# Kernel tuning notes

Hardware: AMD Instinct MI355X
Metric: run time of the kernel (lower is better)

## Reference

```python
import jax, jax.numpy as jnp
import numpy as np

MIN_C = 1e-6
MIN_NORM = 1e-15
BALL_EPS = 0.004  # float32 ball epsilon


def _norm(x):
    return jnp.maximum(jnp.linalg.norm(x, axis=-1, keepdims=True), MIN_NORM)


def _project(x, c):
    norm = _norm(x)
    maxnorm = (1.0 - BALL_EPS) / jnp.sqrt(c)
    return jnp.where(norm > maxnorm, x / norm * maxnorm, x)


def _tanh(x):
    return jnp.tanh(jnp.clip(x, -15.0, 15.0))


def _artanh(x):
    x = jnp.clip(x, -1.0 + 1e-5, 1.0 - 1e-5)
    return 0.5 * (jnp.log1p(x) - jnp.log1p(-x))


def _expmap0(u, c):
    sc = jnp.sqrt(c)
    n = _norm(u)
    return _project(_tanh(sc * n) * u / (sc * n), c)


def _logmap0(y, c):
    sc = jnp.sqrt(c)
    n = _norm(y)
    return y / n / sc * _artanh(sc * n)


def _mobius_add(x, y, c):
    x2 = jnp.sum(x * x, -1, keepdims=True)
    y2 = jnp.sum(y * y, -1, keepdims=True)
    xy = jnp.sum(x * y, -1, keepdims=True)
    num = (1 + 2 * c * xy + c * y2) * x + (1 - c * x2) * y
    den = jnp.maximum(1 + 2 * c * xy + c * c * x2 * y2, MIN_NORM)
    return num / den


N_NODE, N_EDGE, D, ATTN, B, N_VOCAB = 100000, 1000000, 64, 64, 256, 401


def setup_inputs() -> dict:
    key = jax.random.key(0)
    ks = jax.random.split(key, 12)
    r_idx = jax.random.randint(ks[0], (N_EDGE,), 0, B, dtype=jnp.int32)
    rel = jax.random.randint(ks[1], (N_EDGE,), 0, N_VOCAB, dtype=jnp.int32)
    sub = jax.random.randint(ks[2], (N_EDGE,), 0, N_NODE, dtype=jnp.int32)
    obj = jax.random.randint(ks[3], (N_EDGE,), 0, N_NODE, dtype=jnp.int32)
    zero = jnp.zeros((N_EDGE,), jnp.int32)
    edges = jnp.stack([r_idx, zero, rel, zero, sub, obj], axis=1)  # [E, 6]
    s = 0.1
    return {
        "hidden": jax.random.normal(ks[4], (N_NODE, D), jnp.float32) * s,
        "q_rel": jax.random.randint(ks[5], (B,), 0, N_VOCAB, dtype=jnp.int32),
        "edges": edges,
        "rela_embed": jax.random.normal(ks[6], (N_VOCAB, D), jnp.float32) * s,
        "Ws_w": jax.random.normal(ks[7], (ATTN, D), jnp.float32) * s,
        "Wr_w": jax.random.normal(ks[8], (ATTN, D), jnp.float32) * s,
        "Wqr_w": jax.random.normal(ks[9], (ATTN, D), jnp.float32) * s,
        "Wqr_b": jnp.zeros((ATTN,), jnp.float32),
        "Wattn_w": jax.random.normal(ks[10], (1, ATTN), jnp.float32) * s,
        "Wh_w": jax.random.normal(ks[11], (D, D), jnp.float32) * s,
        "n_node": N_NODE,
    }


def reference(hidden, q_rel, edges, rela_embed, Ws_w, Wr_w, Wqr_w, Wqr_b, Wattn_w, Wh_w, n_node):
    c = MIN_C
    sub, rel, obj, r_idx = edges[:, 4], edges[:, 2], edges[:, 5], edges[:, 0]
    hs = hidden[sub]                 # [E, D] gather
    hr = rela_embed[rel]             # [E, D]
    h_qr = rela_embed[q_rel][r_idx]  # [E, D]
    # attention MLP -> scalar gate per edge
    pre = hs @ Ws_w.T + hr @ Wr_w.T + h_qr @ Wqr_w.T + Wqr_b
    alpha = jax.nn.sigmoid(jax.nn.relu(pre) @ Wattn_w.T)  # [E, 1]
    # hyperbolic message
    hs_h = _expmap0(hs, c)
    hr_h = _expmap0(hr, c)
    mess2 = _logmap0(_project(_mobius_add(hs_h, hr_h, c), c), c)
    message = mess2 * alpha
    agg = jax.ops.segment_sum(message, obj, num_segments=n_node)  # scatter-add
    a = _expmap0(agg @ Wh_w.T, c)
    a = jax.nn.relu(a)  # act
    return _logmap0(a, c)
```

## Files before the change

### kernel.cpp

```cpp
#include <hip/hip_runtime.h>
#include <math.h>
#include <stdint.h>

#define N_NODE 100000
#define N_EDGE 1000000
#define DIM    64
#define NB     256
#define NVOCAB 401
#define SCAN_B 1024
#define NCHUNK ((N_NODE + SCAN_B - 1) / SCAN_B)
#define AGG_WAVES 8192

typedef short short8  __attribute__((ext_vector_type(8)));
typedef float floatx4 __attribute__((ext_vector_type(4)));
typedef unsigned short ushort_t;

__device__ inline unsigned short f2bf_rne(float f)
{
    unsigned u = __float_as_uint(f);
    unsigned r = u + 0x7FFF + ((u >> 16) & 1);
    return (unsigned short)(r >> 16);
}
__device__ inline float bflo(unsigned u) { return __uint_as_float(u << 16); }
__device__ inline float bfhi(unsigned u) { return __uint_as_float(u & 0xFFFF0000u); }
__device__ inline unsigned short f2h(float f)
{
    _Float16 h = (_Float16)f;
    unsigned short s; __builtin_memcpy(&s, &h, 2); return s;
}
__device__ inline float h2f(unsigned b)
{
    unsigned short s = (unsigned short)b;
    _Float16 h; __builtin_memcpy(&h, &s, 2); return (float)h;
}

__device__ inline void split8(float4 v0, float4 v1, short8& hi, short8& lo)
{
    float f[8] = {v0.x, v0.y, v0.z, v0.w, v1.x, v1.y, v1.z, v1.w};
    #pragma unroll
    for (int j = 0; j < 8; ++j) {
        unsigned u = __float_as_uint(f[j]);
        unsigned r = u + 0x7FFF + ((u >> 16) & 1);
        unsigned short h = (unsigned short)(r >> 16);
        float hf = __uint_as_float(((unsigned)h) << 16);
        float l  = f[j] - hf;
        unsigned u2 = __float_as_uint(l);
        unsigned r2 = u2 + 0x7FFF + ((u2 >> 16) & 1);
        hi[j] = (short)h;
        lo[j] = (short)(r2 >> 16);
    }
}

__device__ void gemm64_body(
    const float* __restrict__ X,
    const int*   __restrict__ idx,
    const float* __restrict__ W,
    const float* __restrict__ bias,
    void* __restrict__ Yv,
    ushort_t* __restrict__ Y2,
    int R, int out_mode, int blk)
{
    int wave = threadIdx.x >> 6;
    int lane = threadIdx.x & 63;
    int m    = lane & 15;
    int quad = lane >> 4;
    int r0   = blk * 64 + wave * 16;

    int r = r0 + m;
    int src = (r < R) ? (idx ? idx[r] : r) : 0;
    const float* xrow = X + (size_t)src * DIM + quad * 8;

    float4 a0[2], a1[2];
    #pragma unroll
    for (int c = 0; c < 2; ++c) {
        a0[c] = *(const float4*)(xrow + 32 * c);
        a1[c] = *(const float4*)(xrow + 32 * c + 4);
    }
    short8 ah[2], al[2];
    #pragma unroll
    for (int c = 0; c < 2; ++c) split8(a0[c], a1[c], ah[c], al[c]);

    if (out_mode == 3 && r < R) {
        #pragma unroll
        for (int c = 0; c < 2; ++c)
            *(short8*)(Y2 + (size_t)r * DIM + 32 * c + quad * 8) = ah[c];
    }

    floatx4 acc[4] = {{0,0,0,0},{0,0,0,0},{0,0,0,0},{0,0,0,0}};
    #pragma unroll
    for (int g = 0; g < 4; ++g) {
        const float* wrow = W + (size_t)(g * 16 + m) * DIM + quad * 8;
        #pragma unroll
        for (int c = 0; c < 2; ++c) {
            float4 b0 = *(const float4*)(wrow + 32 * c);
            float4 b1 = *(const float4*)(wrow + 32 * c + 4);
            short8 bh, bl;
            split8(b0, b1, bh, bl);
            acc[g] = __builtin_amdgcn_mfma_f32_16x16x32_bf16(ah[c], bh, acc[g], 0, 0, 0);
            acc[g] = __builtin_amdgcn_mfma_f32_16x16x32_bf16(ah[c], bl, acc[g], 0, 0, 0);
            acc[g] = __builtin_amdgcn_mfma_f32_16x16x32_bf16(al[c], bh, acc[g], 0, 0, 0);
        }
    }

    #pragma unroll
    for (int g = 0; g < 4; ++g) {
        float bv = bias ? bias[g * 16 + m] : 0.0f;
        #pragma unroll
        for (int reg = 0; reg < 4; ++reg) {
            int rr = r0 + quad * 4 + reg;
            if (rr < R) {
                float v = acc[g][reg] + bv;
                if (out_mode == 1) v = fmaxf(v, 0.0f);
                if (out_mode >= 2)
                    ((ushort_t*)Yv)[(size_t)rr * DIM + g * 16 + m] = f2bf_rne(v);
                else
                    ((float*)Yv)[(size_t)rr * DIM + g * 16 + m] = v;
            }
        }
    }
}

__global__ __launch_bounds__(256) void gemm64_kernel(
    const float* __restrict__ X,
    const int*   __restrict__ idx,
    const float* __restrict__ W,
    const float* __restrict__ bias,
    void* __restrict__ Yv,
    ushort_t* __restrict__ Y2,
    int R, int out_mode)
{
    gemm64_body(X, idx, W, bias, Yv, Y2, R, out_mode, blockIdx.x);
}

#define G1 ((N_NODE + 63) / 64)
#define G2 ((NVOCAB + 63) / 64)
#define G3 (NB / 64)
#define GSMALL (G2 + G3)
#define GD4 ((N_EDGE + 1023) / 1024)
#define PREP_T (G1 + GD4)
#define PREP_GRID (GSMALL + PREP_T)

__global__ __launch_bounds__(256) void prep_kernel(
    const float* __restrict__ hidden,
    const float* __restrict__ rela,
    const int*   __restrict__ q_rel,
    const float* __restrict__ Ws,
    const float* __restrict__ Wr,
    const float* __restrict__ Wqr,
    const float* __restrict__ Wqr_b,
    ushort_t* __restrict__ hsWs,
    ushort_t* __restrict__ hidb,
    ushort_t* __restrict__ rel_preb,
    ushort_t* __restrict__ relab,
    ushort_t* __restrict__ qr_preb,
    const int* __restrict__ edges,
    int* __restrict__ deg,
    int* __restrict__ rank)
{
    int b = blockIdx.x;
    if (b < G2) {
        gemm64_body(rela, nullptr, Wr, nullptr, rel_preb, relab, NVOCAB, 3, b);
    } else if (b < GSMALL) {
        gemm64_body(rela, q_rel, Wqr, Wqr_b, qr_preb, nullptr, NB, 2, b - G2);
    } else {
        int bp = b - GSMALL;
        int prior = (int)(((long)bp * GD4) / PREP_T);
        int nxt   = (int)(((long)(bp + 1) * GD4) / PREP_T);
        if (nxt > prior) {
            int base = prior * 1024 + threadIdx.x;
            #pragma unroll
            for (int k = 0; k < 4; ++k) {
                int e = base + k * 256;
                if (e < N_EDGE) {
                    int2 so = *(const int2*)(edges + (size_t)e * 6 + 4);
                    rank[e] = atomicAdd(&deg[so.y], 1);
                }
            }
        } else {
            gemm64_body(hidden, nullptr, Ws, nullptr, hsWs, hidb, N_NODE, 3, bp - prior);
        }
    }
}

__global__ __launch_bounds__(SCAN_B) void scan1_kernel(const int* __restrict__ deg,
                                                       int* __restrict__ partial)
{
    __shared__ int s[SCAN_B];
    int g = blockIdx.x * SCAN_B + threadIdx.x;
    s[threadIdx.x] = (g < N_NODE) ? deg[g] : 0;
    __syncthreads();
    for (int off = SCAN_B / 2; off; off >>= 1) {
        if (threadIdx.x < off) s[threadIdx.x] += s[threadIdx.x + off];
        __syncthreads();
    }
    if (threadIdx.x == 0) partial[blockIdx.x] = s[0];
}

__global__ __launch_bounds__(128) void scan2_kernel(int* __restrict__ partial, int n)
{
    __shared__ int s[128];
    int t = threadIdx.x;
    int v = (t < n) ? partial[t] : 0;
    s[t] = v;
    __syncthreads();
    for (int off = 1; off < 128; off <<= 1) {
        int add = (t >= off) ? s[t - off] : 0;
        __syncthreads();
        s[t] += add;
        __syncthreads();
    }
    if (t < n) partial[t] = s[t] - v;
}

__global__ __launch_bounds__(SCAN_B) void scan3_kernel(const int* __restrict__ deg,
                                                       const int* __restrict__ partial,
                                                       int* __restrict__ offs)
{
    __shared__ int s[SCAN_B];
    int g = blockIdx.x * SCAN_B + threadIdx.x;
    s[threadIdx.x] = (g < N_NODE) ? deg[g] : 0;
    __syncthreads();
    for (int off = 1; off < SCAN_B; off <<= 1) {
        int add = ((int)threadIdx.x >= off) ? s[threadIdx.x - off] : 0;
        __syncthreads();
        s[threadIdx.x] += add;
        __syncthreads();
    }
    if (g < N_NODE) {
        offs[g + 1] = partial[blockIdx.x] + s[threadIdx.x];
        if (g == 0) offs[0] = 0;
    }
}

__global__ __launch_bounds__(256) void alpha_scatter_kernel(
    const int*      __restrict__ edges,
    const int*      __restrict__ rank,
    const int*      __restrict__ offs,
    const ushort_t* __restrict__ hsWs,
    const ushort_t* __restrict__ rel_preb,
    const ushort_t* __restrict__ qr_preb,
    const float*    __restrict__ wattn,
    int2*           __restrict__ csr2)
{
    int tid = blockIdx.x * 256 + threadIdx.x;
    if (tid < 4) csr2[N_EDGE + tid] = make_int2(0, 0);

    int wave = threadIdx.x >> 6;
    int lane = threadIdx.x & 63;
    int q    = lane >> 4;
    int l    = lane & 15;
    int f0   = l * 4;
    int e0   = (blockIdx.x * 4 + wave) * 16 + q * 4;

    float4 wa = *(const float4*)(wattn + f0);

    int   sub[4], rl[4], ob[4];
    float t[4];
    #pragma unroll
    for (int j = 0; j < 4; ++j) {
        int e = e0 + j;
        int2 ab = *(const int2*)(edges + (size_t)e * 6);
        int2 cd = *(const int2*)(edges + (size_t)e * 6 + 2);
        int2 ef = *(const int2*)(edges + (size_t)e * 6 + 4);
        rl[j] = cd.x; sub[j] = ef.x; ob[j] = ef.y;

        uint2 uh = *(const uint2*)(hsWs     + (size_t)ef.x * DIM + f0);
        uint2 ur = *(const uint2*)(rel_preb + (size_t)cd.x * DIM + f0);
        uint2 uq = *(const uint2*)(qr_preb  + (size_t)ab.x * DIM + f0);

        float tt =  fmaxf(bflo(uh.x) + bflo(ur.x) + bflo(uq.x), 0.f) * wa.x;
        tt = fmaf(fmaxf(bfhi(uh.x) + bfhi(ur.x) + bfhi(uq.x), 0.f), wa.y, tt);
        tt = fmaf(fmaxf(bflo(uh.y) + bflo(ur.y) + bflo(uq.y), 0.f), wa.z, tt);
        tt = fmaf(fmaxf(bfhi(uh.y) + bfhi(ur.y) + bfhi(uq.y), 0.f), wa.w, tt);
        t[j] = tt;
    }
    #pragma unroll
    for (int j = 0; j < 4; ++j) {
        t[j] += __shfl_xor(t[j], 1);
        t[j] += __shfl_xor(t[j], 2);
        t[j] += __shfl_xor(t[j], 4);
        t[j] += __shfl_xor(t[j], 8);
    }

    if (l == 0) {
        int4 rk = *(const int4*)(rank + e0);
        int rka[4] = {rk.x, rk.y, rk.z, rk.w};
        #pragma unroll
        for (int j = 0; j < 4; ++j) {
            float alpha = 1.0f / (1.0f + __expf(-t[j]));
            int slot = offs[ob[j]] + rka[j];
            csr2[slot] = make_int2(sub[j],
                (int)(((unsigned)rl[j] << 16) | f2h(alpha)));
        }
    }
}

__global__ __launch_bounds__(256) void agg_kernel(
    const int2*     __restrict__ csr2,
    const int*      __restrict__ offs,
    const ushort_t* __restrict__ hB,
    const ushort_t* __restrict__ relab,
    float* __restrict__ out)
{
    int lane = threadIdx.x & 63;
    int q    = lane >> 4;
    int l    = lane & 15;
    int f0   = l * 4;
    int wv = __builtin_amdgcn_readfirstlane((blockIdx.x * blockDim.x + threadIdx.x) >> 6);

    int i   = offs[wv];
    int end = offs[wv + 1];
    for (int n = wv; n < N_NODE; n += AGG_WAVES) {
        int nn = n + AGG_WAVES;
        int ni = 0, ne = 0;
        if (nn < N_NODE) { ni = offs[nn]; ne = offs[nn + 1]; }

        float4 acc = make_float4(0.f, 0.f, 0.f, 0.f);
        int2 e0 = csr2[min(i + q,     N_EDGE + 3)];
        int2 e1 = csr2[min(i + 4 + q, N_EDGE + 3)];
        while (i < end) {
            int2 f0e = csr2[min(i + 8 + q,  N_EDGE + 3)];
            int2 f1e = csr2[min(i + 12 + q, N_EDGE + 3)];
            float v0 = (i + q < end)     ? 1.0f : 0.0f;
            float v1 = (i + 4 + q < end) ? 1.0f : 0.0f;

            unsigned ey0 = (unsigned)e0.y, ey1 = (unsigned)e1.y;
            float al0 = v0 * h2f(ey0 & 0xFFFFu);
            float al1 = v1 * h2f(ey1 & 0xFFFFu);

            uint2 uh0 = *(const uint2*)(hB    + (size_t)e0.x        * DIM + f0);
            uint2 ur0 = *(const uint2*)(relab + (size_t)(ey0 >> 16) * DIM + f0);
            uint2 uh1 = *(const uint2*)(hB    + (size_t)e1.x        * DIM + f0);
            uint2 ur1 = *(const uint2*)(relab + (size_t)(ey1 >> 16) * DIM + f0);

            acc.x = fmaf(al0, bflo(uh0.x) + bflo(ur0.x), acc.x);
            acc.y = fmaf(al0, bfhi(uh0.x) + bfhi(ur0.x), acc.y);
            acc.z = fmaf(al0, bflo(uh0.y) + bflo(ur0.y), acc.z);
            acc.w = fmaf(al0, bfhi(uh0.y) + bfhi(ur0.y), acc.w);
            acc.x = fmaf(al1, bflo(uh1.x) + bflo(ur1.x), acc.x);
            acc.y = fmaf(al1, bfhi(uh1.x) + bfhi(ur1.x), acc.y);
            acc.z = fmaf(al1, bflo(uh1.y) + bflo(ur1.y), acc.z);
            acc.w = fmaf(al1, bfhi(uh1.y) + bfhi(ur1.y), acc.w);

            e0 = f0e; e1 = f1e;
            i += 8;
        }

        acc.x += __shfl_xor(acc.x, 16); acc.x += __shfl_xor(acc.x, 32);
        acc.y += __shfl_xor(acc.y, 16); acc.y += __shfl_xor(acc.y, 32);
        acc.z += __shfl_xor(acc.z, 16); acc.z += __shfl_xor(acc.z, 32);
        acc.w += __shfl_xor(acc.w, 16); acc.w += __shfl_xor(acc.w, 32);
        if (q == 0)
            *(float4*)(out + (size_t)n * DIM + f0) = acc;

        i = ni; end = ne;
    }
}

__global__ __launch_bounds__(256) void edge_kernel(
    const int*      __restrict__ edges,
    const ushort_t* __restrict__ hB,
    const ushort_t* __restrict__ relab,
    const ushort_t* __restrict__ hsWs,
    const ushort_t* __restrict__ rel_preb,
    const ushort_t* __restrict__ qr_preb,
    const float*    __restrict__ wattn,
    float* __restrict__ out)
{
    int e = (blockIdx.x * blockDim.x + threadIdx.x) >> 6;
    if (e >= N_EDGE) return;
    int lane = threadIdx.x & 63;
    int r_i = edges[e * 6 + 0];
    int rl  = edges[e * 6 + 2];
    int sb  = edges[e * 6 + 4];
    int ob  = edges[e * 6 + 5];
    float hs = __uint_as_float(((unsigned)hB[(size_t)sb * DIM + lane]) << 16);
    float hr = __uint_as_float(((unsigned)relab[(size_t)rl * DIM + lane]) << 16);
    float p1 = __uint_as_float(((unsigned)hsWs[(size_t)sb * DIM + lane]) << 16);
    float p2 = __uint_as_float(((unsigned)rel_preb[(size_t)rl * DIM + lane]) << 16);
    float p3 = __uint_as_float(((unsigned)qr_preb[(size_t)r_i * DIM + lane]) << 16);
    float t = wattn[lane] * fmaxf(p1 + p2 + p3, 0.0f);
    #pragma unroll
    for (int off = 32; off; off >>= 1) t += __shfl_xor(t, off);
    float alpha = 1.0f / (1.0f + __expf(-t));
    atomicAdd(&out[(size_t)ob * DIM + lane], (hs + hr) * alpha);
}

extern "C" void kernel_launch(void* const* d_in, const int* in_sizes, int n_in,
                              void* d_out, int out_size, void* d_ws, size_t ws_size,
                              hipStream_t stream)
{
    const float* hidden = (const float*)d_in[0];
    const int*   q_rel  = (const int*)  d_in[1];
    const int*   edges  = (const int*)  d_in[2];
    const float* rela   = (const float*)d_in[3];
    const float* Ws     = (const float*)d_in[4];
    const float* Wr     = (const float*)d_in[5];
    const float* Wqr    = (const float*)d_in[6];
    const float* Wqr_b  = (const float*)d_in[7];
    const float* Wattn  = (const float*)d_in[8];
    const float* Wh     = (const float*)d_in[9];
    float* out = (float*)d_out;

    ushort_t* qr_preb  = (ushort_t*)d_ws;
    ushort_t* rel_preb = qr_preb + NB * DIM;
    ushort_t* relab    = rel_preb + NVOCAB * DIM;
    ushort_t* hsWs     = relab + NVOCAB * DIM;
    ushort_t* hidb     = hsWs + (size_t)N_NODE * DIM;
    int* rank    = (int*)(hidb + (size_t)N_NODE * DIM);
    int* deg     = rank + N_EDGE;
    int* offs    = deg + N_NODE;
    int* partial = offs + (N_NODE + 1);
    int* csr_raw = partial + 128;
    int2* csr2   = (int2*)(((uintptr_t)csr_raw + 7) & ~(uintptr_t)7);
    size_t csr_need = ((char*)csr2 - (char*)d_ws) + (size_t)(N_EDGE + 4) * sizeof(int2);
    bool use_csr = ws_size >= csr_need;

    if (use_csr) {
        hipMemsetAsync(deg, 0, N_NODE * sizeof(int), stream);
        prep_kernel<<<PREP_GRID, 256, 0, stream>>>(
            hidden, rela, q_rel, Ws, Wr, Wqr, Wqr_b,
            hsWs, hidb, rel_preb, relab, qr_preb, edges, deg, rank);
        scan1_kernel<<<NCHUNK, SCAN_B, 0, stream>>>(deg, partial);
        scan2_kernel<<<1, 128, 0, stream>>>(partial, NCHUNK);
        scan3_kernel<<<NCHUNK, SCAN_B, 0, stream>>>(deg, partial, offs);
        alpha_scatter_kernel<<<N_EDGE / 64, 256, 0, stream>>>(
            edges, rank, offs, hsWs, rel_preb, qr_preb, Wattn, csr2);
        agg_kernel<<<AGG_WAVES / 4, 256, 0, stream>>>(csr2, offs, hidb, relab, out);
    } else {
        gemm64_kernel<<<(NVOCAB + 63) / 64, 256, 0, stream>>>(
            rela, nullptr, Wr, nullptr, rel_preb, relab, NVOCAB, 3);
        gemm64_kernel<<<(NB + 63) / 64, 256, 0, stream>>>(
            rela, q_rel, Wqr, Wqr_b, qr_preb, nullptr, NB, 2);
        gemm64_kernel<<<(N_NODE + 63) / 64, 256, 0, stream>>>(
            hidden, nullptr, Ws, nullptr, hsWs, hidb, N_NODE, 3);
        hipMemsetAsync(d_out, 0, (size_t)N_NODE * DIM * sizeof(float), stream);
        edge_kernel<<<(N_EDGE + 3) / 4, 256, 0, stream>>>(
            edges, hidb, relab, hsWs, rel_preb, qr_preb, Wattn, out);
    }

    gemm64_kernel<<<(N_NODE + 63) / 64, 256, 0, stream>>>(
        out, nullptr, Wh, nullptr, out, nullptr, N_NODE, 1);
}
```

Baseline: 265.9 us.

## Shard degree atomics, pack edge indices, and store aggregate as bf16

Degree counting is split across 8 shards keyed by edge block, so atomics on the same destination node collide less. The scan kernels now also write per-shard base offsets for the scatter step. Prep packs sub/rel/obj/r_idx into an 8-byte int2 per edge, so the alpha-scatter pass reads less than the 24-byte edge rows. The aggregate is written as bf16 and fed to a new bf16-A MFMA GEMM for Wh. This cuts memory traffic at some precision cost and uses more workspace for the sharded degree array.

```diff
diff --git a/kernel.cpp b/kernel.cpp
--- a/kernel.cpp
+++ b/kernel.cpp
@@ -10,6 +10,8 @@
 #define SCAN_B 1024
 #define NCHUNK ((N_NODE + SCAN_B - 1) / SCAN_B)
 #define AGG_WAVES 8192
+#define NSHARD 8
+#define EPB 2048
 
 typedef short short8  __attribute__((ext_vector_type(8)));
 typedef float floatx4 __attribute__((ext_vector_type(4)));
@@ -121,23 +123,63 @@
 }
 
 __global__ __launch_bounds__(256) void gemm64_kernel(
-    const float* __restrict__ X,
-    const int*   __restrict__ idx,
+    const float* __restrict__ X, const int* __restrict__ idx,
+    const float* __restrict__ W, const float* __restrict__ bias,
+    void* __restrict__ Yv, ushort_t* __restrict__ Y2, int R, int out_mode)
+{
+    gemm64_body(X, idx, W, bias, Yv, Y2, R, out_mode, blockIdx.x);
+}
+
+__global__ __launch_bounds__(256) void gemm64_bf16A_kernel(
+    const ushort_t* __restrict__ A,
     const float* __restrict__ W,
-    const float* __restrict__ bias,
-    void* __restrict__ Yv,
-    ushort_t* __restrict__ Y2,
-    int R, int out_mode)
-{
-    gemm64_body(X, idx, W, bias, Yv, Y2, R, out_mode, blockIdx.x);
+    float* __restrict__ Y, int R)
+{
+    int wave = threadIdx.x >> 6;
+    int lane = threadIdx.x & 63;
+    int m    = lane & 15;
+    int quad = lane >> 4;
+    int r0   = blockIdx.x * 64 + wave * 16;
+
+    int r = r0 + m;
+    int src = (r < R) ? r : 0;
+    short8 a8[2];
+    #pragma unroll
+    for (int c = 0; c < 2; ++c)
+        a8[c] = *(const short8*)(A + (size_t)src * DIM + 32 * c + quad * 8);
+
+    floatx4 acc[4] = {{0,0,0,0},{0,0,0,0},{0,0,0,0},{0,0,0,0}};
+    #pragma unroll
+    for (int g = 0; g < 4; ++g) {
+        const float* wrow = W + (size_t)(g * 16 + m) * DIM + quad * 8;
+        #pragma unroll
+        for (int c = 0; c < 2; ++c) {
+            float4 b0 = *(const float4*)(wrow + 32 * c);
+            float4 b1 = *(const float4*)(wrow + 32 * c + 4);
+            short8 bh, bl;
+            split8(b0, b1, bh, bl);
+            acc[g] = __builtin_amdgcn_mfma_f32_16x16x32_bf16(a8[c], bh, acc[g], 0, 0, 0);
+            acc[g] = __builtin_amdgcn_mfma_f32_16x16x32_bf16(a8[c], bl, acc[g], 0, 0, 0);
+        }
+    }
+
+    #pragma unroll
+    for (int g = 0; g < 4; ++g) {
+        #pragma unroll
+        for (int reg = 0; reg < 4; ++reg) {
+            int rr = r0 + quad * 4 + reg;
+            if (rr < R)
+                Y[(size_t)rr * DIM + g * 16 + m] = fmaxf(acc[g][reg], 0.0f);
+        }
+    }
 }
 
 #define G1 ((N_NODE + 63) / 64)
 #define G2 ((NVOCAB + 63) / 64)
 #define G3 (NB / 64)
 #define GSMALL (G2 + G3)
-#define GD4 ((N_EDGE + 1023) / 1024)
-#define PREP_T (G1 + GD4)
+#define GD8 ((N_EDGE + EPB - 1) / EPB)
+#define PREP_T (G1 + GD8)
 #define PREP_GRID (GSMALL + PREP_T)
 
 __global__ __launch_bounds__(256) void prep_kernel(
@@ -154,8 +196,9 @@
     ushort_t* __restrict__ relab,
     ushort_t* __restrict__ qr_preb,
     const int* __restrict__ edges,
-    int* __restrict__ deg,
-    int* __restrict__ rank)
+    int* __restrict__ deg8,
+    int* __restrict__ rank,
+    int2* __restrict__ epack)
 {
     int b = blockIdx.x;
     if (b < G2) {
@@ -164,16 +207,20 @@
         gemm64_body(rela, q_rel, Wqr, Wqr_b, qr_preb, nullptr, NB, 2, b - G2);
     } else {
         int bp = b - GSMALL;
-        int prior = (int)(((long)bp * GD4) / PREP_T);
-        int nxt   = (int)(((long)(bp + 1) * GD4) / PREP_T);
+        int prior = (int)(((long)bp * GD8) / PREP_T);
+        int nxt   = (int)(((long)(bp + 1) * GD8) / PREP_T);
         if (nxt > prior) {
-            int base = prior * 1024 + threadIdx.x;
+            int base = prior * EPB + threadIdx.x;
             #pragma unroll
-            for (int k = 0; k < 4; ++k) {
+            for (int k = 0; k < 8; ++k) {
                 int e = base + k * 256;
                 if (e < N_EDGE) {
-                    int2 so = *(const int2*)(edges + (size_t)e * 6 + 4);
-                    rank[e] = atomicAdd(&deg[so.y], 1);
+                    int2 ab = *(const int2*)(edges + (size_t)e * 6);
+                    int2 cd = *(const int2*)(edges + (size_t)e * 6 + 2);
+                    int2 ef = *(const int2*)(edges + (size_t)e * 6 + 4);
+                    epack[e] = make_int2(ef.x | (cd.x << 17), ef.y | (ab.x << 17));
+                    int s = (e >> 11) & (NSHARD - 1);
+                    rank[e] = atomicAdd(&deg8[s * N_NODE + ef.y], 1);
                 }
             }
         } else {
@@ -182,12 +229,16 @@
     }
 }
 
-__global__ __launch_bounds__(SCAN_B) void scan1_kernel(const int* __restrict__ deg,
+__global__ __launch_bounds__(SCAN_B) void scan1_kernel(const int* __restrict__ deg8,
                                                        int* __restrict__ partial)
 {
     __shared__ int s[SCAN_B];
     int g = blockIdx.x * SCAN_B + threadIdx.x;
-    s[threadIdx.x] = (g < N_NODE) ? deg[g] : 0;
+    int tot = 0;
+    if (g < N_NODE)
+        #pragma unroll
+        for (int k = 0; k < NSHARD; ++k) tot += deg8[k * N_NODE + g];
+    s[threadIdx.x] = tot;
     __syncthreads();
     for (int off = SCAN_B / 2; off; off >>= 1) {
         if (threadIdx.x < off) s[threadIdx.x] += s[threadIdx.x + off];
@@ -212,13 +263,19 @@
     if (t < n) partial[t] = s[t] - v;
 }
 
-__global__ __launch_bounds__(SCAN_B) void scan3_kernel(const int* __restrict__ deg,
+__global__ __launch_bounds__(SCAN_B) void scan3_kernel(int* __restrict__ deg8,
                                                        const int* __restrict__ partial,
                                                        int* __restrict__ offs)
 {
     __shared__ int s[SCAN_B];
     int g = blockIdx.x * SCAN_B + threadIdx.x;
-    s[threadIdx.x] = (g < N_NODE) ? deg[g] : 0;
+    int d[NSHARD];
+    int tot = 0;
+    if (g < N_NODE) {
+        #pragma unroll
+        for (int k = 0; k < NSHARD; ++k) { d[k] = deg8[k * N_NODE + g]; tot += d[k]; }
+    }
+    s[threadIdx.x] = tot;
     __syncthreads();
     for (int off = 1; off < SCAN_B; off <<= 1) {
         int add = ((int)threadIdx.x >= off) ? s[threadIdx.x - off] : 0;
@@ -227,15 +284,19 @@
         __syncthreads();
     }
     if (g < N_NODE) {
-        offs[g + 1] = partial[blockIdx.x] + s[threadIdx.x];
+        int incl = partial[blockIdx.x] + s[threadIdx.x];
+        offs[g + 1] = incl;
         if (g == 0) offs[0] = 0;
+        int run = incl - tot;
+        #pragma unroll
+        for (int k = 0; k < NSHARD; ++k) { deg8[k * N_NODE + g] = run; run += d[k]; }
     }
 }
 
 __global__ __launch_bounds__(256) void alpha_scatter_kernel(
-    const int*      __restrict__ edges,
+    const int2*     __restrict__ epack,
     const int*      __restrict__ rank,
-    const int*      __restrict__ offs,
+    const int*      __restrict__ base8,
     const ushort_t* __restrict__ hsWs,
     const ushort_t* __restrict__ rel_preb,
     const ushort_t* __restrict__ qr_preb,
@@ -259,14 +320,15 @@
     #pragma unroll
     for (int j = 0; j < 4; ++j) {
         int e = e0 + j;
-        int2 ab = *(const int2*)(edges + (size_t)e * 6);
-        int2 cd = *(const int2*)(edges + (size_t)e * 6 + 2);
-        int2 ef = *(const int2*)(edges + (size_t)e * 6 + 4);
-        rl[j] = cd.x; sub[j] = ef.x; ob[j] = ef.y;
-
-        uint2 uh = *(const uint2*)(hsWs     + (size_t)ef.x * DIM + f0);
-        uint2 ur = *(const uint2*)(rel_preb + (size_t)cd.x * DIM + f0);
-        uint2 uq = *(const uint2*)(qr_preb  + (size_t)ab.x * DIM + f0);
+        int2 ep = epack[e];
+        sub[j] = ep.x & 0x1FFFF;
+        rl[j]  = (int)((unsigned)ep.x >> 17);
+        ob[j]  = ep.y & 0x1FFFF;
+        int ri = (int)((unsigned)ep.y >> 17);
+
+        uint2 uh = *(const uint2*)(hsWs     + (size_t)sub[j] * DIM + f0);
+        uint2 ur = *(const uint2*)(rel_preb + (size_t)rl[j]  * DIM + f0);
+        uint2 uq = *(const uint2*)(qr_preb  + (size_t)ri     * DIM + f0);
 
         float tt =  fmaxf(bflo(uh.x) + bflo(ur.x) + bflo(uq.x), 0.f) * wa.x;
         tt = fmaf(fmaxf(bfhi(uh.x) + bfhi(ur.x) + bfhi(uq.x), 0.f), wa.y, tt);
@@ -285,10 +347,11 @@
     if (l == 0) {
         int4 rk = *(const int4*)(rank + e0);
         int rka[4] = {rk.x, rk.y, rk.z, rk.w};
+        int sh = (e0 >> 11) & (NSHARD - 1);
         #pragma unroll
         for (int j = 0; j < 4; ++j) {
             float alpha = 1.0f / (1.0f + __expf(-t[j]));
-            int slot = offs[ob[j]] + rka[j];
+            int slot = base8[sh * N_NODE + ob[j]] + rka[j];
             csr2[slot] = make_int2(sub[j],
                 (int)(((unsigned)rl[j] << 16) | f2h(alpha)));
         }
@@ -300,7 +363,7 @@
     const int*      __restrict__ offs,
     const ushort_t* __restrict__ hB,
     const ushort_t* __restrict__ relab,
-    float* __restrict__ out)
+    ushort_t* __restrict__ aggb)
 {
     int lane = threadIdx.x & 63;
     int q    = lane >> 4;
@@ -350,8 +413,12 @@
         acc.y += __shfl_xor(acc.y, 16); acc.y += __shfl_xor(acc.y, 32);
         acc.z += __shfl_xor(acc.z, 16); acc.z += __shfl_xor(acc.z, 32);
         acc.w += __shfl_xor(acc.w, 16); acc.w += __shfl_xor(acc.w, 32);
-        if (q == 0)
-            *(float4*)(out + (size_t)n * DIM + f0) = acc;
+        if (q == 0) {
+            uint2 o;
+            o.x = (unsigned)f2bf_rne(acc.x) | ((unsigned)f2bf_rne(acc.y) << 16);
+            o.y = (unsigned)f2bf_rne(acc.z) | ((unsigned)f2bf_rne(acc.w) << 16);
+            *(uint2*)(aggb + (size_t)n * DIM + f0) = o;
+        }
 
         i = ni; end = ne;
     }
@@ -407,26 +474,28 @@
     ushort_t* relab    = rel_preb + NVOCAB * DIM;
     ushort_t* hsWs     = relab + NVOCAB * DIM;
     ushort_t* hidb     = hsWs + (size_t)N_NODE * DIM;
-    int* rank    = (int*)(hidb + (size_t)N_NODE * DIM);
-    int* deg     = rank + N_EDGE;
-    int* offs    = deg + N_NODE;
-    int* partial = offs + (N_NODE + 1);
-    int* csr_raw = partial + 128;
-    int2* csr2   = (int2*)(((uintptr_t)csr_raw + 7) & ~(uintptr_t)7);
-    size_t csr_need = ((char*)csr2 - (char*)d_ws) + (size_t)(N_EDGE + 4) * sizeof(int2);
+    int2* epack  = (int2*)(((uintptr_t)(hidb + (size_t)N_NODE * DIM) + 15) & ~(uintptr_t)15);
+    int*  rank   = (int*)(epack + N_EDGE);
+    int*  deg8   = rank + N_EDGE;
+    int*  offs   = deg8 + NSHARD * N_NODE;
+    int*  partial= offs + (N_NODE + 1);
+    int2* csr2   = (int2*)(((uintptr_t)(partial + 128) + 15) & ~(uintptr_t)15);
+    size_t csr_need = ((char*)(csr2 + N_EDGE + 4)) - (char*)d_ws;
     bool use_csr = ws_size >= csr_need;
+    ushort_t* aggb = (ushort_t*)epack;
 
     if (use_csr) {
-        hipMemsetAsync(deg, 0, N_NODE * sizeof(int), stream);
+        hipMemsetAsync(deg8, 0, NSHARD * N_NODE * sizeof(int), stream);
         prep_kernel<<<PREP_GRID, 256, 0, stream>>>(
             hidden, rela, q_rel, Ws, Wr, Wqr, Wqr_b,
-            hsWs, hidb, rel_preb, relab, qr_preb, edges, deg, rank);
-        scan1_kernel<<<NCHUNK, SCAN_B, 0, stream>>>(deg, partial);
+            hsWs, hidb, rel_preb, relab, qr_preb, edges, deg8, rank, epack);
+        scan1_kernel<<<NCHUNK, SCAN_B, 0, stream>>>(deg8, partial);
         scan2_kernel<<<1, 128, 0, stream>>>(partial, NCHUNK);
-        scan3_kernel<<<NCHUNK, SCAN_B, 0, stream>>>(deg, partial, offs);
+        scan3_kernel<<<NCHUNK, SCAN_B, 0, stream>>>(deg8, partial, offs);
         alpha_scatter_kernel<<<N_EDGE / 64, 256, 0, stream>>>(
-            edges, rank, offs, hsWs, rel_preb, qr_preb, Wattn, csr2);
-        agg_kernel<<<AGG_WAVES / 4, 256, 0, stream>>>(csr2, offs, hidb, relab, out);
+            epack, rank, deg8, hsWs, rel_preb, qr_preb, Wattn, csr2);
+        agg_kernel<<<AGG_WAVES / 4, 256, 0, stream>>>(csr2, offs, hidb, relab, aggb);
+        gemm64_bf16A_kernel<<<(N_NODE + 63) / 64, 256, 0, stream>>>(aggb, Wh, out, N_NODE);
     } else {
         gemm64_kernel<<<(NVOCAB + 63) / 64, 256, 0, stream>>>(
             rela, nullptr, Wr, nullptr, rel_preb, relab, NVOCAB, 3);
@@ -437,8 +506,7 @@
         hipMemsetAsync(d_out, 0, (size_t)N_NODE * DIM * sizeof(float), stream);
         edge_kernel<<<(N_EDGE + 3) / 4, 256, 0, stream>>>(
             edges, hidb, relab, hsWs, rel_preb, qr_preb, Wattn, out);
-    }
-
-    gemm64_kernel<<<(N_NODE + 63) / 64, 256, 0, stream>>>(
-        out, nullptr, Wh, nullptr, out, nullptr, N_NODE, 1);
-}
+        gemm64_kernel<<<(N_NODE + 63) / 64, 256, 0, stream>>>(
+            out, nullptr, Wh, nullptr, out, nullptr, N_NODE, 1);
+    }
+}
```

Result: faster. 258.0 us (-3.0%).
